# Performance work log

Measured on AMD Instinct MI355X. Metric: run time of the kernel, lower is better.

The kernel has to match this reference:

```python
import jax, jax.numpy as jnp
import numpy as np

NUM_HEADS = 16
EMBED = 1024
BLOCK = 2048
VOCAB = 32000
HEAD = EMBED // NUM_HEADS


def setup_inputs() -> dict:
    key = jax.random.key(0)
    ks = jax.random.split(key, 9)
    B, T = 2, 2048
    x = jax.random.randint(ks[0], (B, T), 0, VOCAB)
    target = jax.random.randint(ks[1], (B, T), 0, VOCAB)
    s = 0.02
    tok_emb = jax.random.normal(ks[2], (VOCAB, EMBED), jnp.float32) * s
    pos_emb = jax.random.normal(ks[3], (BLOCK, EMBED), jnp.float32) * s
    Wq = jax.random.normal(ks[4], (EMBED, EMBED), jnp.float32) * s
    Wk = jax.random.normal(ks[5], (EMBED, EMBED), jnp.float32) * s
    Wv = jax.random.normal(ks[6], (EMBED, EMBED), jnp.float32) * s
    W_lm = jax.random.normal(ks[7], (EMBED, VOCAB), jnp.float32) * s
    b_lm = jnp.zeros((VOCAB,), jnp.float32)
    return {"x": x, "target": target, "tok_emb": tok_emb, "pos_emb": pos_emb,
            "Wq": Wq, "Wk": Wk, "Wv": Wv, "W_lm": W_lm, "b_lm": b_lm}


def reference(x, target, tok_emb, pos_emb, Wq, Wk, Wv, W_lm, b_lm):
    B, T = x.shape
    h = tok_emb[x] + pos_emb[:T]                       # [B,T,E]
    # fused QKV projections, then split into heads (equivalent to per-head Linears + concat)
    q = (h @ Wq).reshape(B, T, NUM_HEADS, HEAD)
    k = (h @ Wk).reshape(B, T, NUM_HEADS, HEAD)
    v = (h @ Wv).reshape(B, T, NUM_HEADS, HEAD)
    scores = jnp.einsum("bqhd,bkhd->bhqk", q, k) / (HEAD ** 0.5)
    causal = jnp.tril(jnp.ones((T, T), bool))
    scores = jnp.where(causal, scores, -jnp.inf)
    attn = jax.nn.softmax(scores, axis=-1)             # [B,H,T,T]
    out = jnp.einsum("bhqk,bkhd->bqhd", attn, v).reshape(B, T, EMBED)
    logits = out @ W_lm + b_lm                         # [B,T,V]
    logits_flat = logits.reshape(B * T, VOCAB)
    logp = jax.nn.log_softmax(logits_flat, axis=-1)
    loss = -jnp.take_along_axis(logp, target.reshape(-1, 1), axis=-1).mean()
    return logits_flat, loss
```

## Files before the change

kernel.cpp:

```cpp
#include <hip/hip_runtime.h>
#include <cstdint>
#include <cstddef>

#define EMB   1024
#define TSEQ  2048
#define NBATCH 2
#define NHEAD 16
#define HDIM  64
#define VOCAB 32000
#define ROWS  4096
#define NCB   125

typedef __attribute__((ext_vector_type(8))) short short8;
typedef __attribute__((ext_vector_type(4))) float f32x4;

__device__ __forceinline__ unsigned short f2bf(float f) {
  unsigned int u = __float_as_uint(f);
  u = (u + 0x7FFFu + ((u >> 16) & 1u)) >> 16;
  return (unsigned short)u;
}

__device__ __forceinline__ void gload16(const void* g, void* l) {
  typedef __attribute__((address_space(1))) const unsigned int gu;
  typedef __attribute__((address_space(3))) unsigned int lu;
  __builtin_amdgcn_global_load_lds((gu*)g, (lu*)l, 16, 0, 0);
}

__global__ void convT(const float* __restrict__ in, unsigned short* __restrict__ out,
                      int R, int C) {
  __shared__ float tile[32][33];
  const int ct = blockIdx.x, rt = blockIdx.y;
  const int t = threadIdx.x;
  const int r0 = t >> 5;
  const int c  = t & 31;
#pragma unroll
  for (int i = 0; i < 4; ++i) {
    int r = r0 + i * 8;
    tile[r][c] = in[(size_t)(rt * 32 + r) * C + ct * 32 + c];
  }
  __syncthreads();
#pragma unroll
  for (int i = 0; i < 4; ++i) {
    int r = r0 + i * 8;
    out[(size_t)(ct * 32 + r) * R + rt * 32 + c] = f2bf(tile[c][r]);
  }
}

__global__ void embed_kernel(const int* __restrict__ x, const float* __restrict__ tok,
                             const float* __restrict__ pos, unsigned short* __restrict__ h) {
  const int idx = blockIdx.x * 256 + threadIdx.x;
  const int row = idx >> 8;
  const int c4  = idx & 255;
  const int tpos = row & (TSEQ - 1);
  const int token = x[row];
  float4 a = *(const float4*)(tok + (size_t)token * EMB + c4 * 4);
  float4 p = *(const float4*)(pos + (size_t)tpos * EMB + c4 * 4);
  unsigned int lo = (unsigned int)f2bf(a.x + p.x) | ((unsigned int)f2bf(a.y + p.y) << 16);
  unsigned int hi = (unsigned int)f2bf(a.z + p.z) | ((unsigned int)f2bf(a.w + p.w) << 16);
  *(uint2*)(h + (size_t)idx * 4) = make_uint2(lo, hi);
}

__global__ void gemm_qkv(const unsigned short* __restrict__ A,
                         const unsigned short* __restrict__ Bt,
                         unsigned short* __restrict__ Qo,
                         unsigned short* __restrict__ Ko,
                         unsigned short* __restrict__ Vto) {
  __shared__ unsigned short As[2][128 * 32];
  __shared__ unsigned short Bs[2][128 * 32];
  const int K = EMB;
  const int t  = threadIdx.x;
  const int l  = t & 63;
  const int w  = t >> 6;
  const int wr = w >> 1, wc = w & 1;
  const int m0 = blockIdx.y * 128;
  const int n0 = blockIdx.x * 128;
  const int KT = K >> 5;

  f32x4 acc[4][4] = {};

  const int crow = t >> 2;
  const int coff = (t & 3) * 16;
  const size_t abase = ((size_t)(m0 + crow) * K) * 2 + coff;
  const size_t bbase = ((size_t)(n0 + crow) * K) * 2 + coff;
  const size_t rstep = (size_t)64 * K * 2;
  const char* Ab = (const char*)A;
  const char* Bb = (const char*)Bt;

#define STAGE(buf, kt_) do {                                              \
    size_t ko = (size_t)(kt_) * 64;                                       \
    gload16(Ab + abase + ko,         (char*)&As[(buf)][0] + t * 16);      \
    gload16(Ab + abase + rstep + ko, (char*)&As[(buf)][0] + t * 16 + 4096);\
    gload16(Bb + bbase + ko,         (char*)&Bs[(buf)][0] + t * 16);      \
    gload16(Bb + bbase + rstep + ko, (char*)&Bs[(buf)][0] + t * 16 + 4096);\
  } while (0)

  const int lr  = l & 15;
  const int lkb = (l >> 4) * 16;

#define COMPUTE(buf) do {                                                  \
    const char* ab = (const char*)&As[(buf)][0];                           \
    const char* bb = (const char*)&Bs[(buf)][0];                           \
    short8 fa[4], fb[4];                                                   \
    _Pragma("unroll")                                                      \
    for (int m = 0; m < 4; ++m)                                            \
      fa[m] = *(const short8*)(ab + (wr * 64 + m * 16 + lr) * 64 + lkb);   \
    _Pragma("unroll")                                                      \
    for (int n = 0; n < 4; ++n)                                            \
      fb[n] = *(const short8*)(bb + (wc * 64 + n * 16 + lr) * 64 + lkb);   \
    _Pragma("unroll")                                                      \
    for (int m = 0; m < 4; ++m)                                            \
      _Pragma("unroll")                                                    \
      for (int n = 0; n < 4; ++n)                                          \
        acc[m][n] = __builtin_amdgcn_mfma_f32_16x16x32_bf16(               \
            fa[m], fb[n], acc[m][n], 0, 0, 0);                             \
  } while (0)

  STAGE(0, 0);
  __syncthreads();
  int cur = 0;
  for (int kt = 0; kt < KT; ++kt) {
    if (kt + 1 < KT) STAGE(cur ^ 1, kt + 1);
    COMPUTE(cur);
    __syncthreads();
    cur ^= 1;
  }
#undef STAGE
#undef COMPUTE

  const int sec = n0 >> 10;
  const int orow = m0 + wr * 64 + (l >> 4) * 4;
  const int ocol = n0 + wc * 64 + lr;
#pragma unroll
  for (int m = 0; m < 4; ++m) {
#pragma unroll
    for (int n = 0; n < 4; ++n) {
      const int col = ocol + n * 16;
      const int c10 = col & 1023;
      if (sec == 0) {
#pragma unroll
        for (int r = 0; r < 4; ++r)
          Qo[(size_t)(orow + m * 16 + r) * EMB + c10] = f2bf(acc[m][n][r] * 0.125f);
      } else if (sec == 1) {
#pragma unroll
        for (int r = 0; r < 4; ++r)
          Ko[(size_t)(orow + m * 16 + r) * EMB + c10] = f2bf(acc[m][n][r]);
      } else {
        int row0 = orow + m * 16;
        int bb_ = row0 >> 11, tq = row0 & 2047;
        int hh = c10 >> 6, dd = c10 & 63;
        unsigned int lo = (unsigned int)f2bf(acc[m][n][0]) | ((unsigned int)f2bf(acc[m][n][1]) << 16);
        unsigned int hi = (unsigned int)f2bf(acc[m][n][2]) | ((unsigned int)f2bf(acc[m][n][3]) << 16);
        *(uint2*)&Vto[(((size_t)(bb_ * NHEAD + hh) * HDIM + dd) * TSEQ) + tq] = make_uint2(lo, hi);
      }
    }
  }
}

__global__ __launch_bounds__(256)
void attn_mfma(const unsigned short* __restrict__ Qbf,
               const unsigned short* __restrict__ Kbf,
               const unsigned short* __restrict__ Vtbf,
               unsigned short* __restrict__ Obf) {
  const int qt = (gridDim.x - 1) - blockIdx.x;
  const int h  = blockIdx.y;
  const int b  = blockIdx.z;
  const int t  = threadIdx.x, w = t >> 6, l = t & 63;
  const int g  = l >> 4, c = l & 15;
  const int qw = qt * 64 + w * 16;
  const int qg = qw + c;

  __shared__ unsigned short Ks[2][32 * 64];
  __shared__ unsigned short Vs[2][64 * 32];

  const unsigned short* Qrow = Qbf + ((size_t)(b * TSEQ + qg) * EMB + h * HDIM);
  short8 qfrag[2];
  qfrag[0] = *(const short8*)(Qrow + g * 8);
  qfrag[1] = *(const short8*)(Qrow + g * 8 + 32);

  f32x4 accO[4] = {};
  float mrun = -3e38f, lsum = 0.0f;

  const int kvt = t >> 3, kch = t & 7;
  const char* Kg = (const char*)(Kbf + ((size_t)(b * TSEQ + kvt) * EMB + h * HDIM))
                   + (((kch * 16) ^ ((kvt & 7) << 4)));
  const int dt = t >> 2, vch = t & 3;
  const char* Vg = (const char*)(Vtbf + (((size_t)(b * NHEAD + h) * HDIM + dt) * TSEQ))
                   + vch * 16;
  const size_t kstep = (size_t)32 * EMB * 2;
  const size_t vstep = (size_t)32 * 2;

#define ASTAGE(buf, kt_) do {                                               \
    gload16(Kg + (size_t)(kt_) * kstep, (char*)&Ks[buf][0] + t * 16);       \
    gload16(Vg + (size_t)(kt_) * vstep, (char*)&Vs[buf][0] + t * 16);       \
  } while (0)

  const int nkt = 2 * qt + 2;
  ASTAGE(0, 0);
  __syncthreads();
  int cur = 0;
  for (int kt = 0; kt < nkt; ++kt) {
    if (kt + 1 < nkt) ASTAGE(cur ^ 1, kt + 1);
    const int k0 = kt * 32;

    const char* kb = (const char*)&Ks[cur][0];
    f32x4 sa[2] = {};
#pragma unroll
    for (int kc = 0; kc < 2; ++kc) {
#pragma unroll
      for (int kh = 0; kh < 2; ++kh) {
        short8 ka = *(const short8*)(kb + (kc * 16 + c) * 128 +
                                     ((g * 16 + kh * 64) ^ ((c & 7) << 4)));
        sa[kc] = __builtin_amdgcn_mfma_f32_16x16x32_bf16(ka, qfrag[kh], sa[kc], 0, 0, 0);
      }
    }

    float sv[8];
#pragma unroll
    for (int kc = 0; kc < 2; ++kc)
#pragma unroll
      for (int r = 0; r < 4; ++r) {
        int kv = k0 + kc * 16 + g * 4 + r;
        sv[kc * 4 + r] = (kv > qg) ? -3e38f : sa[kc][r];
      }
    float pm = sv[0];
#pragma unroll
    for (int i = 1; i < 8; ++i) pm = fmaxf(pm, sv[i]);
    pm = fmaxf(pm, __shfl_xor(pm, 16));
    pm = fmaxf(pm, __shfl_xor(pm, 32));
    const float mnew = fmaxf(mrun, pm);
    const float alpha = __expf(mrun - mnew);
    float ps = 0.0f;
#pragma unroll
    for (int i = 0; i < 8; ++i) { float p = __expf(sv[i] - mnew); sv[i] = p; ps += p; }
    ps += __shfl_xor(ps, 16);
    ps += __shfl_xor(ps, 32);
    lsum = lsum * alpha + ps;
    mrun = mnew;

#pragma unroll
    for (int r = 0; r < 4; ++r) {
      float ar = __shfl(alpha, g * 4 + r);
      accO[0][r] *= ar; accO[1][r] *= ar; accO[2][r] *= ar; accO[3][r] *= ar;
    }

    unsigned int wf[4];
#pragma unroll
    for (int rp = 0; rp < 2; ++rp)
#pragma unroll
      for (int kc = 0; kc < 2; ++kc) {
        unsigned int rw;
        asm("v_cvt_pk_bf16_f32 %0, %1, %2"
            : "=v"(rw) : "v"(sv[kc * 4 + 2 * rp]), "v"(sv[kc * 4 + 2 * rp + 1]));
        wf[rp * 2 + kc] = rw;
      }

    union { unsigned int u[4]; short8 s8; } pa;
#pragma unroll
    for (int jp = 0; jp < 4; ++jp) {
      int srcLane = c + ((2 * (g & 1) + (jp >> 1)) << 4);
      unsigned int v0 = (unsigned int)__shfl((int)wf[2 * (jp & 1)], srcLane);
      unsigned int v1 = (unsigned int)__shfl((int)wf[2 * (jp & 1) + 1], srcLane);
      pa.u[jp] = (g >> 1) ? v1 : v0;
    }

    const char* vb = (const char*)&Vs[cur][0];
#pragma unroll
    for (int cp = 0; cp < 4; ++cp) {
      short8 vf = *(const short8*)(vb + (c + 16 * cp) * 64 + g * 16);
      accO[cp] = __builtin_amdgcn_mfma_f32_16x16x32_bf16(pa.s8, vf, accO[cp], 0, 0, 0);
    }

    __syncthreads();
    cur ^= 1;
  }
#undef ASTAGE

  const float inv = 1.0f / lsum;
#pragma unroll
  for (int r = 0; r < 4; ++r) {
    float ir = __shfl(inv, g * 4 + r);
    unsigned short* orow = Obf + ((size_t)(b * TSEQ + qw + g * 4 + r) * EMB + h * HDIM);
#pragma unroll
    for (int cp = 0; cp < 4; ++cp)
      orow[c + 16 * cp] = f2bf(accO[cp][r] * ir);
  }
}

__global__ __launch_bounds__(512, 2)
void gemm_lm(const unsigned short* __restrict__ A,
             const unsigned short* __restrict__ Bt,
             const float* __restrict__ bias,
             float* __restrict__ C,
             float* __restrict__ pm, float* __restrict__ ps) {
  extern __shared__ char lds[];
  const int t = threadIdx.x;
  const int w = t >> 6, l = t & 63;
  const int wm = w >> 2, wn = w & 3;
  const int fr = l & 15, kg = l >> 4;

  const int L  = blockIdx.x;
  const int Lp = (L & 7) * 250 + (L >> 3);
  const int g_ = Lp / 500;
  const int q_ = Lp % 500;
  const int ntile = q_ >> 2;
  const int mtile = g_ * 4 + (q_ & 3);

  const char* Ag = (const char*)A;
  const char* Bg = (const char*)Bt;

  const int srow = t >> 3;
  const int scl  = t & 7;
  const int scg  = scl ^ (srow & 7);
  size_t aoff0 = ((size_t)(mtile * 256 +       srow) * EMB) * 2 + scg * 16;
  size_t aoff1 = ((size_t)(mtile * 256 + 128 + srow) * EMB) * 2 + scg * 16;
  size_t boff0 = ((size_t)(ntile * 256 +       srow) * EMB) * 2 + scg * 16;
  size_t boff1 = ((size_t)(ntile * 256 + 128 + srow) * EMB) * 2 + scg * 16;

#define STG_A(buf_, kt_, ah_) do {                                          \
    char* d = lds + (buf_) * 65536 + (ah_) * 16384 + t * 16;                \
    const char* s = Ag + ((ah_) ? aoff1 : aoff0) + (size_t)(kt_) * 128;     \
    gload16(s, d); gload16(s + 131072, d + 8192);                           \
  } while (0)
#define STG_B(buf_, kt_, bh_) do {                                          \
    char* d = lds + (buf_) * 65536 + 32768 + (bh_) * 16384 + t * 16;        \
    const char* s = Bg + ((bh_) ? boff1 : boff0) + (size_t)(kt_) * 128;     \
    gload16(s, d); gload16(s + 131072, d + 8192);                           \
  } while (0)

  const int xr  = fr & 7;
  const int cb0 = (kg ^ xr) * 16;
  const int arow = (wm * 128 + fr) * 128;
  const int brow = (wn * 64 + fr) * 128;

  f32x4 acc[8][4] = {};
  short8 fa[4][2], fb[4][2];

#define MFMA_Q(MH, NH)                                                       \
  _Pragma("unroll")                                                          \
  for (int mi = 0; mi < 4; ++mi)                                             \
    _Pragma("unroll")                                                        \
    for (int ni = 0; ni < 2; ++ni)                                           \
      _Pragma("unroll")                                                      \
      for (int ks = 0; ks < 2; ++ks)                                         \
        acc[(MH)*4+mi][(NH)*2+ni] = __builtin_amdgcn_mfma_f32_16x16x32_bf16( \
            fa[mi][ks], fb[(NH)*2+ni][ks], acc[(MH)*4+mi][(NH)*2+ni], 0,0,0);

#define TILE(h_, S1, S2, VMN) do {                                           \
    const int buf_ = (h_) & 1;                                               \
    char* Abase = lds + buf_ * 65536;                                        \
    char* Bbase = Abase + 32768;                                             \
                                                            \
    _Pragma("unroll")                                                        \
    for (int mi = 0; mi < 4; ++mi) {                                         \
      fa[mi][0] = *(const short8*)(Abase + arow + mi*2048 + cb0);            \
      fa[mi][1] = *(const short8*)(Abase + arow + mi*2048 + (cb0^64));       \
    }                                                                        \
    _Pragma("unroll")                                                        \
    for (int ni = 0; ni < 2; ++ni) {                                         \
      fb[ni][0] = *(const short8*)(Bbase + brow + ni*2048 + cb0);            \
      fb[ni][1] = *(const short8*)(Bbase + brow + ni*2048 + (cb0^64));       \
    }                                                                        \
    if (S1) STG_A(buf_^1, (h_)+1, 0);                                        \
    __builtin_amdgcn_s_barrier();                                            \
    __builtin_amdgcn_s_setprio(1); MFMA_Q(0,0); __builtin_amdgcn_s_setprio(0);\
    __builtin_amdgcn_s_barrier();                                            \
                                                            \
    _Pragma("unroll")                                                        \
    for (int ni = 0; ni < 2; ++ni) {                                         \
      fb[2+ni][0] = *(const short8*)(Bbase + brow + (2+ni)*2048 + cb0);      \
      fb[2+ni][1] = *(const short8*)(Bbase + brow + (2+ni)*2048 + (cb0^64));  \
    }                                                                        \
    if (S1) STG_A(buf_^1, (h_)+1, 1);                                        \
    __builtin_amdgcn_s_barrier();                                            \
    __builtin_amdgcn_s_setprio(1); MFMA_Q(0,1); __builtin_amdgcn_s_setprio(0);\
    __builtin_amdgcn_s_barrier();                                            \
                                                            \
    _Pragma("unroll")                                                        \
    for (int mi = 0; mi < 4; ++mi) {                                         \
      fa[mi][0] = *(const short8*)(Abase + arow + (4+mi)*2048 + cb0);        \
      fa[mi][1] = *(const short8*)(Abase + arow + (4+mi)*2048 + (cb0^64));   \
    }                                                                        \
    if (S2) STG_B(buf_, (h_)+2, 0);                                          \
    __builtin_amdgcn_s_barrier();                                            \
    __builtin_amdgcn_s_setprio(1); MFMA_Q(1,1); __builtin_amdgcn_s_setprio(0);\
    __builtin_amdgcn_s_barrier();                                            \
                                                            \
    if (S2) STG_B(buf_, (h_)+2, 1);                                          \
    __builtin_amdgcn_s_barrier();                                            \
    __builtin_amdgcn_s_setprio(1); MFMA_Q(1,0); __builtin_amdgcn_s_setprio(0);\
    if (VMN) asm volatile("s_waitcnt vmcnt(4)" ::: "memory");                \
    else     asm volatile("s_waitcnt vmcnt(0)" ::: "memory");                \
    __builtin_amdgcn_s_barrier();                                            \
  } while (0)

  STG_B(0, 0, 0); STG_B(0, 0, 1); STG_A(0, 0, 0); STG_A(0, 0, 1);
  STG_B(1, 1, 0); STG_B(1, 1, 1);
  asm volatile("s_waitcnt vmcnt(4)" ::: "memory");
  __builtin_amdgcn_s_barrier();

  for (int h = 0; h < 14; ++h) TILE(h, 1, 1, 4);
  TILE(14, 1, 0, 0);
  TILE(15, 0, 0, 0);
#undef TILE
#undef MFMA_Q
#undef STG_A
#undef STG_B

  __syncthreads();

  const int mrow0 = mtile * 256 + wm * 128;
  const int ncol0 = ntile * 256 + wn * 64;
  float biasv[4];
#pragma unroll
  for (int ni = 0; ni < 4; ++ni) biasv[ni] = bias[ncol0 + ni * 16 + fr];
#pragma unroll
  for (int mi = 0; mi < 8; ++mi)
#pragma unroll
    for (int ni = 0; ni < 4; ++ni)
#pragma unroll
      for (int rr = 0; rr < 4; ++rr)
        acc[mi][ni][rr] += biasv[ni];

#pragma unroll
  for (int mi = 0; mi < 8; ++mi)
#pragma unroll
    for (int rr = 0; rr < 4; ++rr) {
      int row = mrow0 + mi * 16 + kg * 4 + rr;
      float* cr = C + (size_t)row * VOCAB + ncol0 + fr;
#pragma unroll
      for (int ni = 0; ni < 4; ++ni) cr[ni * 16] = acc[mi][ni][rr];
    }

  float* redm = (float*)lds;
  float* reds = (float*)(lds + 4096);
#pragma unroll
  for (int mi = 0; mi < 8; ++mi)
#pragma unroll
    for (int rr = 0; rr < 4; ++rr) {
      float m1 = fmaxf(fmaxf(acc[mi][0][rr], acc[mi][1][rr]),
                       fmaxf(acc[mi][2][rr], acc[mi][3][rr]));
      m1 = fmaxf(m1, __shfl_xor(m1, 1));
      m1 = fmaxf(m1, __shfl_xor(m1, 2));
      m1 = fmaxf(m1, __shfl_xor(m1, 4));
      m1 = fmaxf(m1, __shfl_xor(m1, 8));
      if (fr == 0) redm[(wm * 4 + wn) * 128 + mi * 16 + kg * 4 + rr] = m1;
    }
  __syncthreads();

  float rmx[8][4];
#pragma unroll
  for (int mi = 0; mi < 8; ++mi)
#pragma unroll
    for (int rr = 0; rr < 4; ++rr) {
      int row = mi * 16 + kg * 4 + rr;
      float a0 = fmaxf(redm[(wm*4+0)*128 + row], redm[(wm*4+1)*128 + row]);
      float a1 = fmaxf(redm[(wm*4+2)*128 + row], redm[(wm*4+3)*128 + row]);
      rmx[mi][rr] = fmaxf(a0, a1);
    }
#pragma unroll
  for (int mi = 0; mi < 8; ++mi)
#pragma unroll
    for (int rr = 0; rr < 4; ++rr) {
      float r = rmx[mi][rr];
      float s1 = __expf(acc[mi][0][rr] - r) + __expf(acc[mi][1][rr] - r)
               + __expf(acc[mi][2][rr] - r) + __expf(acc[mi][3][rr] - r);
      s1 += __shfl_xor(s1, 1);
      s1 += __shfl_xor(s1, 2);
      s1 += __shfl_xor(s1, 4);
      s1 += __shfl_xor(s1, 8);
      if (fr == 0) reds[(wm * 4 + wn) * 128 + mi * 16 + kg * 4 + rr] = s1;
    }
  __syncthreads();

  if (wn == 0 && fr == 0) {
#pragma unroll
    for (int mi = 0; mi < 8; ++mi)
#pragma unroll
      for (int rr = 0; rr < 4; ++rr) {
        int row = mi * 16 + kg * 4 + rr;
        float ssum = reds[(wm*4+0)*128 + row] + reds[(wm*4+1)*128 + row]
                   + reds[(wm*4+2)*128 + row] + reds[(wm*4+3)*128 + row];
        int grow = mrow0 + row;
        pm[(size_t)grow * NCB + ntile] = rmx[mi][rr];
        ps[(size_t)grow * NCB + ntile] = ssum;
      }
  }
}

__global__ void loss_rows2(const float* __restrict__ pm, const float* __restrict__ ps,
                           const float* __restrict__ logits, const int* __restrict__ tgt,
                           float* __restrict__ partial) {
  const int row = blockIdx.x * 4 + (threadIdx.x >> 6);
  const int l = threadIdx.x & 63;
  const float* pmr = pm + (size_t)row * NCB;
  const float* psr = ps + (size_t)row * NCB;
  float m = -3e38f, s = 0.0f;
  for (int i = l; i < NCB; i += 64) {
    float mv = pmr[i], sv = psr[i];
    float nm = fmaxf(m, mv);
    s = s * __expf(m - nm) + sv * __expf(mv - nm);
    m = nm;
  }
#pragma unroll
  for (int off = 1; off < 64; off <<= 1) {
    float om = __shfl_xor(m, off), os = __shfl_xor(s, off);
    float nm = fmaxf(m, om);
    s = s * __expf(m - nm) + os * __expf(om - nm);
    m = nm;
  }
  if (l == 0) {
    float lse = m + __logf(s);
    partial[row] = -(logits[(size_t)row * VOCAB + tgt[row]] - lse);
  }
}

__global__ void loss_final(const float* __restrict__ partial, float* __restrict__ out) {
  const int t = threadIdx.x;
  float s = 0.0f;
  for (int i = t; i < ROWS; i += 256) s += partial[i];
#pragma unroll
  for (int off = 1; off < 64; off <<= 1) s += __shfl_xor(s, off);
  __shared__ float ws_[4];
  if ((t & 63) == 0) ws_[t >> 6] = s;
  __syncthreads();
  if (t == 0) out[0] = (ws_[0] + ws_[1] + ws_[2] + ws_[3]) * (1.0f / (float)ROWS);
}

extern "C" void kernel_launch(void* const* d_in, const int* in_sizes, int n_in,
                              void* d_out, int out_size, void* d_ws, size_t ws_size,
                              hipStream_t stream) {
  const int*   x      = (const int*)d_in[0];
  const int*   target = (const int*)d_in[1];
  const float* tok    = (const float*)d_in[2];
  const float* pos    = (const float*)d_in[3];
  const float* Wq     = (const float*)d_in[4];
  const float* Wk     = (const float*)d_in[5];
  const float* Wv     = (const float*)d_in[6];
  const float* Wlm    = (const float*)d_in[7];
  const float* blm    = (const float*)d_in[8];
  float* out = (float*)d_out;

  char* p = (char*)d_ws;
  unsigned short* Wqt  = (unsigned short*)p; p += (size_t)EMB * EMB * 2;
  unsigned short* Wkt  = (unsigned short*)p; p += (size_t)EMB * EMB * 2;
  unsigned short* Wvt  = (unsigned short*)p; p += (size_t)EMB * EMB * 2;
  unsigned short* Wlmt = (unsigned short*)p; p += (size_t)VOCAB * EMB * 2;
  unsigned short* hbf  = (unsigned short*)p; p += (size_t)ROWS * EMB * 2;
  unsigned short* qbf  = (unsigned short*)p; p += (size_t)ROWS * EMB * 2;
  unsigned short* kbf  = (unsigned short*)p; p += (size_t)ROWS * EMB * 2;
  unsigned short* vtbf = (unsigned short*)p; p += (size_t)ROWS * EMB * 2;
  unsigned short* obf  = (unsigned short*)p; p += (size_t)ROWS * EMB * 2;
  float*          prt  = (float*)p;          p += (size_t)ROWS * 4;
  float*          pmw  = (float*)p;          p += (size_t)ROWS * NCB * 4;
  float*          psw  = (float*)p;          p += (size_t)ROWS * NCB * 4;

  (void)hipFuncSetAttribute((const void*)gemm_lm,
                            hipFuncAttributeMaxDynamicSharedMemorySize, 131072);

  dim3 b256(256);
  convT<<<dim3(EMB / 32, EMB / 32), b256, 0, stream>>>(Wq, Wqt, EMB, EMB);
  convT<<<dim3(EMB / 32, EMB / 32), b256, 0, stream>>>(Wk, Wkt, EMB, EMB);
  convT<<<dim3(EMB / 32, EMB / 32), b256, 0, stream>>>(Wv, Wvt, EMB, EMB);
  convT<<<dim3(VOCAB / 32, EMB / 32), b256, 0, stream>>>(Wlm, Wlmt, EMB, VOCAB);

  embed_kernel<<<ROWS * (EMB / 4) / 256, b256, 0, stream>>>(x, tok, pos, hbf);

  gemm_qkv<<<dim3(3 * EMB / 128, ROWS / 128), b256, 0, stream>>>(hbf, Wqt, qbf, kbf, vtbf);

  attn_mfma<<<dim3(TSEQ / 64, NHEAD, NBATCH), b256, 0, stream>>>(qbf, kbf, vtbf, obf);

  gemm_lm<<<dim3((ROWS / 256) * (VOCAB / 256)), dim3(512), 131072, stream>>>(
      obf, Wlmt, blm, out, pmw, psw);

  loss_rows2<<<ROWS / 4, b256, 0, stream>>>(pmw, psw, out, target, prt);
  loss_final<<<1, b256, 0, stream>>>(prt, out + (size_t)ROWS * VOCAB);
}
```

Measured before the change: 620.9 us.

## Process two 16-row query groups per wave in attention to reuse K/V tiles

Each attention workgroup now covers 128 query rows instead of 64, and each wave handles two 16-row groups that share the same K and V fragments read from LDS. This halves the number of K/V tile loads from global memory into LDS per query and raises MFMA work per LDS read. In exchange it halves the grid size, which hurts load balance on the causal triangle. It also raises register use (double accumulators and running max/sum) and wastes more masked work on the diagonal tiles.

```diff
diff --git a/kernel.cpp b/kernel.cpp
--- a/kernel.cpp
+++ b/kernel.cpp
@@ -166,19 +166,22 @@
   const int b  = blockIdx.z;
   const int t  = threadIdx.x, w = t >> 6, l = t & 63;
   const int g  = l >> 4, c = l & 15;
-  const int qw = qt * 64 + w * 16;
-  const int qg = qw + c;
+  const int qw = qt * 128 + w * 32;
 
   __shared__ unsigned short Ks[2][32 * 64];
   __shared__ unsigned short Vs[2][64 * 32];
 
-  const unsigned short* Qrow = Qbf + ((size_t)(b * TSEQ + qg) * EMB + h * HDIM);
-  short8 qfrag[2];
-  qfrag[0] = *(const short8*)(Qrow + g * 8);
-  qfrag[1] = *(const short8*)(Qrow + g * 8 + 32);
-
-  f32x4 accO[4] = {};
-  float mrun = -3e38f, lsum = 0.0f;
+  short8 qfrag[2][2];
+#pragma unroll
+  for (int G = 0; G < 2; ++G) {
+    const unsigned short* Qrow =
+        Qbf + ((size_t)(b * TSEQ + qw + G * 16 + c) * EMB + h * HDIM);
+    qfrag[G][0] = *(const short8*)(Qrow + g * 8);
+    qfrag[G][1] = *(const short8*)(Qrow + g * 8 + 32);
+  }
+
+  f32x4 accO[2][4] = {};
+  float mrun[2] = {-3e38f, -3e38f}, lsum[2] = {0.0f, 0.0f};
 
   const int kvt = t >> 3, kch = t & 7;
   const char* Kg = (const char*)(Kbf + ((size_t)(b * TSEQ + kvt) * EMB + h * HDIM))
@@ -194,7 +197,7 @@
     gload16(Vg + (size_t)(kt_) * vstep, (char*)&Vs[buf][0] + t * 16);       \
   } while (0)
 
-  const int nkt = 2 * qt + 2;
+  const int nkt = 4 * qt + 4;
   ASTAGE(0, 0);
   __syncthreads();
   int cur = 0;
@@ -203,71 +206,80 @@
     const int k0 = kt * 32;
 
     const char* kb = (const char*)&Ks[cur][0];
-    f32x4 sa[2] = {};
+    f32x4 sa[2][2] = {};
 #pragma unroll
     for (int kc = 0; kc < 2; ++kc) {
 #pragma unroll
       for (int kh = 0; kh < 2; ++kh) {
         short8 ka = *(const short8*)(kb + (kc * 16 + c) * 128 +
                                      ((g * 16 + kh * 64) ^ ((c & 7) << 4)));
-        sa[kc] = __builtin_amdgcn_mfma_f32_16x16x32_bf16(ka, qfrag[kh], sa[kc], 0, 0, 0);
+        sa[0][kc] = __builtin_amdgcn_mfma_f32_16x16x32_bf16(ka, qfrag[0][kh], sa[0][kc], 0, 0, 0);
+        sa[1][kc] = __builtin_amdgcn_mfma_f32_16x16x32_bf16(ka, qfrag[1][kh], sa[1][kc], 0, 0, 0);
       }
     }
 
-    float sv[8];
-#pragma unroll
-    for (int kc = 0; kc < 2; ++kc)
+    const char* vb = (const char*)&Vs[cur][0];
+    short8 vf[4];
+#pragma unroll
+    for (int cp = 0; cp < 4; ++cp)
+      vf[cp] = *(const short8*)(vb + (c + 16 * cp) * 64 + g * 16);
+
+#pragma unroll
+    for (int G = 0; G < 2; ++G) {
+      const int qg = qw + G * 16 + c;
+      float sv[8];
+#pragma unroll
+      for (int kc = 0; kc < 2; ++kc)
+#pragma unroll
+        for (int r = 0; r < 4; ++r) {
+          int kv = k0 + kc * 16 + g * 4 + r;
+          sv[kc * 4 + r] = (kv > qg) ? -3e38f : sa[G][kc][r];
+        }
+      float pm = sv[0];
+#pragma unroll
+      for (int i = 1; i < 8; ++i) pm = fmaxf(pm, sv[i]);
+      pm = fmaxf(pm, __shfl_xor(pm, 16));
+      pm = fmaxf(pm, __shfl_xor(pm, 32));
+      const float mnew = fmaxf(mrun[G], pm);
+      const float alpha = __expf(mrun[G] - mnew);
+      float ps = 0.0f;
+#pragma unroll
+      for (int i = 0; i < 8; ++i) { float p = __expf(sv[i] - mnew); sv[i] = p; ps += p; }
+      ps += __shfl_xor(ps, 16);
+      ps += __shfl_xor(ps, 32);
+      lsum[G] = lsum[G] * alpha + ps;
+      mrun[G] = mnew;
+
 #pragma unroll
       for (int r = 0; r < 4; ++r) {
-        int kv = k0 + kc * 16 + g * 4 + r;
-        sv[kc * 4 + r] = (kv > qg) ? -3e38f : sa[kc][r];
+        float ar = __shfl(alpha, g * 4 + r);
+        accO[G][0][r] *= ar; accO[G][1][r] *= ar;
+        accO[G][2][r] *= ar; accO[G][3][r] *= ar;
       }
-    float pm = sv[0];
-#pragma unroll
-    for (int i = 1; i < 8; ++i) pm = fmaxf(pm, sv[i]);
-    pm = fmaxf(pm, __shfl_xor(pm, 16));
-    pm = fmaxf(pm, __shfl_xor(pm, 32));
-    const float mnew = fmaxf(mrun, pm);
-    const float alpha = __expf(mrun - mnew);
-    float ps = 0.0f;
-#pragma unroll
-    for (int i = 0; i < 8; ++i) { float p = __expf(sv[i] - mnew); sv[i] = p; ps += p; }
-    ps += __shfl_xor(ps, 16);
-    ps += __shfl_xor(ps, 32);
-    lsum = lsum * alpha + ps;
-    mrun = mnew;
-
-#pragma unroll
-    for (int r = 0; r < 4; ++r) {
-      float ar = __shfl(alpha, g * 4 + r);
-      accO[0][r] *= ar; accO[1][r] *= ar; accO[2][r] *= ar; accO[3][r] *= ar;
-    }
-
-    unsigned int wf[4];
-#pragma unroll
-    for (int rp = 0; rp < 2; ++rp)
-#pragma unroll
-      for (int kc = 0; kc < 2; ++kc) {
-        unsigned int rw;
-        asm("v_cvt_pk_bf16_f32 %0, %1, %2"
-            : "=v"(rw) : "v"(sv[kc * 4 + 2 * rp]), "v"(sv[kc * 4 + 2 * rp + 1]));
-        wf[rp * 2 + kc] = rw;
+
+      unsigned int wf[4];
+#pragma unroll
+      for (int rp = 0; rp < 2; ++rp)
+#pragma unroll
+        for (int kc = 0; kc < 2; ++kc) {
+          unsigned int rw;
+          asm("v_cvt_pk_bf16_f32 %0, %1, %2"
+              : "=v"(rw) : "v"(sv[kc * 4 + 2 * rp]), "v"(sv[kc * 4 + 2 * rp + 1]));
+          wf[rp * 2 + kc] = rw;
+        }
+
+      union { unsigned int u[4]; short8 s8; } pa;
+#pragma unroll
+      for (int jp = 0; jp < 4; ++jp) {
+        int srcLane = c + ((2 * (g & 1) + (jp >> 1)) << 4);
+        unsigned int v0 = (unsigned int)__shfl((int)wf[2 * (jp & 1)], srcLane);
+        unsigned int v1 = (unsigned int)__shfl((int)wf[2 * (jp & 1) + 1], srcLane);
+        pa.u[jp] = (g >> 1) ? v1 : v0;
       }
 
-    union { unsigned int u[4]; short8 s8; } pa;
-#pragma unroll
-    for (int jp = 0; jp < 4; ++jp) {
-      int srcLane = c + ((2 * (g & 1) + (jp >> 1)) << 4);
-      unsigned int v0 = (unsigned int)__shfl((int)wf[2 * (jp & 1)], srcLane);
-      unsigned int v1 = (unsigned int)__shfl((int)wf[2 * (jp & 1) + 1], srcLane);
-      pa.u[jp] = (g >> 1) ? v1 : v0;
-    }
-
-    const char* vb = (const char*)&Vs[cur][0];
-#pragma unroll
-    for (int cp = 0; cp < 4; ++cp) {
-      short8 vf = *(const short8*)(vb + (c + 16 * cp) * 64 + g * 16);
-      accO[cp] = __builtin_amdgcn_mfma_f32_16x16x32_bf16(pa.s8, vf, accO[cp], 0, 0, 0);
+#pragma unroll
+      for (int cp = 0; cp < 4; ++cp)
+        accO[G][cp] = __builtin_amdgcn_mfma_f32_16x16x32_bf16(pa.s8, vf[cp], accO[G][cp], 0, 0, 0);
     }
 
     __syncthreads();
@@ -275,14 +287,18 @@
   }
 #undef ASTAGE
 
-  const float inv = 1.0f / lsum;
-#pragma unroll
-  for (int r = 0; r < 4; ++r) {
-    float ir = __shfl(inv, g * 4 + r);
-    unsigned short* orow = Obf + ((size_t)(b * TSEQ + qw + g * 4 + r) * EMB + h * HDIM);
-#pragma unroll
-    for (int cp = 0; cp < 4; ++cp)
-      orow[c + 16 * cp] = f2bf(accO[cp][r] * ir);
+#pragma unroll
+  for (int G = 0; G < 2; ++G) {
+    const float inv = 1.0f / lsum[G];
+#pragma unroll
+    for (int r = 0; r < 4; ++r) {
+      float ir = __shfl(inv, g * 4 + r);
+      unsigned short* orow =
+          Obf + ((size_t)(b * TSEQ + qw + G * 16 + g * 4 + r) * EMB + h * HDIM);
+#pragma unroll
+      for (int cp = 0; cp < 4; ++cp)
+        orow[c + 16 * cp] = f2bf(accO[G][cp][r] * ir);
+    }
   }
 }
 
@@ -567,7 +583,7 @@
 
   gemm_qkv<<<dim3(3 * EMB / 128, ROWS / 128), b256, 0, stream>>>(hbf, Wqt, qbf, kbf, vtbf);
 
-  attn_mfma<<<dim3(TSEQ / 64, NHEAD, NBATCH), b256, 0, stream>>>(qbf, kbf, vtbf, obf);
+  attn_mfma<<<dim3(TSEQ / 128, NHEAD, NBATCH), b256, 0, stream>>>(qbf, kbf, vtbf, obf);
 
   gemm_lm<<<dim3((ROWS / 256) * (VOCAB / 256)), dim3(512), 131072, stream>>>(
       obf, Wlmt, blm, out, pmw, psw);
```

After: 622.9 us. No clear change (+0.3%).
